# Optimization experiments

Hardware: AMD Instinct MI355X
Metric: run time of the kernel (lower is better)

## Reference

```python
import jax, jax.numpy as jnp
import numpy as np

B, T, F, H, BN = 131072, 20, 5, 32, 16


def _lstm_layer(x, Wih, Whh, bih, bhh):
    # x: [B, T, I]; Wih: [4H, I]; Whh: [4H, H]; biases: [4H]
    # PyTorch gate order: i, f, g, o
    b, h = x.shape[0], Whh.shape[1]
    x_t = jnp.swapaxes(x, 0, 1)                              # [T, B, I]
    pre = jnp.einsum('tbi,gi->tbg', x_t, Wih) + bih + bhh    # input contribution precomputed

    def step(carry, p):
        hprev, cprev = carry
        z = p + hprev @ Whh.T                                # [B, 4H]
        i, f, g, o = jnp.split(z, 4, axis=-1)
        i = jax.nn.sigmoid(i); f = jax.nn.sigmoid(f)
        g = jnp.tanh(g);       o = jax.nn.sigmoid(o)
        c = f * cprev + i * g
        hh = o * jnp.tanh(c)
        return (hh, c), hh

    h0 = jnp.zeros((b, h), x.dtype)
    (hT, cT), hs = jax.lax.scan(step, (h0, h0), pre)
    return jnp.swapaxes(hs, 0, 1), hT                        # [B, T, H], [B, H]


def setup_inputs() -> dict:
    key = jax.random.key(0)
    ks = jax.random.split(key, 24)
    k = 1.0 / np.sqrt(H)
    u = lambda kk, shp: jax.random.uniform(kk, shp, jnp.float32, -k, k)
    d = {
        'x': jax.random.normal(ks[0], (B, T, F), jnp.float32),
        # encoder layer 0 (input F) and layer 1 (input H)
        'enc_Wih0': u(ks[1], (4 * H, F)),  'enc_Whh0': u(ks[2], (4 * H, H)),
        'enc_bih0': u(ks[3], (4 * H,)),    'enc_bhh0': u(ks[4], (4 * H,)),
        'enc_Wih1': u(ks[5], (4 * H, H)),  'enc_Whh1': u(ks[6], (4 * H, H)),
        'enc_bih1': u(ks[7], (4 * H,)),    'enc_bhh1': u(ks[8], (4 * H,)),
        # bottleneck / expand MLPs
        'bn_W': u(ks[9], (BN, H)),  'bn_b': u(ks[10], (BN,)),
        'ex_W': u(ks[11], (H, BN)), 'ex_b': u(ks[12], (H,)),
        # decoder layers (both input H)
        'dec_Wih0': u(ks[13], (4 * H, H)), 'dec_Whh0': u(ks[14], (4 * H, H)),
        'dec_bih0': u(ks[15], (4 * H,)),   'dec_bhh0': u(ks[16], (4 * H,)),
        'dec_Wih1': u(ks[17], (4 * H, H)), 'dec_Whh1': u(ks[18], (4 * H, H)),
        'dec_bih1': u(ks[19], (4 * H,)),   'dec_bhh1': u(ks[20], (4 * H,)),
        # output projection
        'out_W': u(ks[21], (F, H)), 'out_b': u(ks[22], (F,)),
    }
    return d


def reference(x, enc_Wih0, enc_Whh0, enc_bih0, enc_bhh0,
              enc_Wih1, enc_Whh1, enc_bih1, enc_bhh1,
              bn_W, bn_b, ex_W, ex_b,
              dec_Wih0, dec_Whh0, dec_bih0, dec_bhh0,
              dec_Wih1, dec_Whh1, dec_bih1, dec_bhh1,
              out_W, out_b):
    # encoder (dropout inactive at inference)
    h0_seq, _ = _lstm_layer(x, enc_Wih0, enc_Whh0, enc_bih0, enc_bhh0)
    _, last_hidden = _lstm_layer(h0_seq, enc_Wih1, enc_Whh1, enc_bih1, enc_bhh1)
    latent = jax.nn.relu(last_hidden @ bn_W.T + bn_b)        # [B, BN]
    expanded = jax.nn.relu(latent @ ex_W.T + ex_b)           # [B, H]
    dec_in = jnp.broadcast_to(expanded[:, None, :], (expanded.shape[0], T, H))
    d0_seq, _ = _lstm_layer(dec_in, dec_Wih0, dec_Whh0, dec_bih0, dec_bhh0)
    d1_seq, _ = _lstm_layer(d0_seq, dec_Wih1, dec_Whh1, dec_bih1, dec_bhh1)
    return jnp.einsum('bth,fh->btf', d1_seq, out_W) + out_b  # [B, T, F]
```

## Files before the change

kernel.cpp:

```cpp
#include <hip/hip_runtime.h>

typedef float    f32x4 __attribute__((ext_vector_type(4)));
typedef _Float16 f16x8 __attribute__((ext_vector_type(8)));

#define BATCH 131072
#define SEQT  20
#define L1F  1.4426950408889634f
#define L2F  2.8853900817779268f

__device__ __forceinline__ float fexp2(float x){ return __builtin_amdgcn_exp2f(x); }
__device__ __forceinline__ float frcp (float x){ return __builtin_amdgcn_rcpf(x); }

__device__ __forceinline__ f32x4 MFMA(f16x8 a, f16x8 b, f32x4 c){
  return __builtin_amdgcn_mfma_f32_16x16x32_f16(a, b, c, 0, 0, 0);
}
__device__ __forceinline__ f16x8 zero8h(){
  f16x8 z;
#pragma unroll
  for (int e=0;e<8;++e) z[e]=(_Float16)0.f;
  return z;
}

__device__ __forceinline__ f16x8 pack8h(f32x4 lo, f32x4 hi, float sc){
  f16x8 f;
#pragma unroll
  for (int e=0;e<4;++e){ f[e] = (_Float16)(sc*lo[e]); f[4+e] = (_Float16)(sc*hi[e]); }
  return f;
}
__device__ __forceinline__ f16x8 gfragH(const float* __restrict__ W, int row, int kg, float sc){
  f32x4 lo = *(const f32x4*)(W + row*32 + 4*kg);
  f32x4 hi = *(const f32x4*)(W + row*32 + 16 + 4*kg);
  return pack8h(lo, hi, sc);
}
__device__ __forceinline__ f32x4 ld4(const float* __restrict__ p){ return *(const f32x4*)p; }

__device__ __forceinline__ void activate(const f32x4* acc, float* cs, f16x8& ph){
  float hv[8];
#pragma unroll
  for (int mm=0; mm<2; ++mm)
#pragma unroll
  for (int r=0; r<4; ++r){
    const int e = mm*4 + r;
    float zi = acc[0+mm][r];
    float zf = acc[2+mm][r];
    float zg = acc[4+mm][r];
    float zo = acc[6+mm][r];
    float A  = fexp2(-zi);
    float F  = fexp2(-zf);
    float B  = fexp2(zg);
    float ab = (1.0f+A)*(B+1.0f);
    float fp = 1.0f+F;
    float r1 = frcp(ab*fp);
    float cn = fmaf(ab*r1, cs[e], (B-1.0f)*fp*r1);
    cs[e] = cn;
    float E  = fexp2(-zo);
    float D  = fexp2(L2F*cn);
    hv[e] = (D-1.0f)*frcp((1.0f+E)*(D+1.0f));
  }
  f16x8 P;
#pragma unroll
  for (int e=0;e<8;++e) P[e] = (_Float16)hv[e];
  ph = P;
}

__global__ __launch_bounds__(256, 3) void lstm_ae_mfma(
    const float* __restrict__ x,
    const float* __restrict__ eWih0, const float* __restrict__ eWhh0,
    const float* __restrict__ ebih0, const float* __restrict__ ebhh0,
    const float* __restrict__ eWih1, const float* __restrict__ eWhh1,
    const float* __restrict__ ebih1, const float* __restrict__ ebhh1,
    const float* __restrict__ bnW,   const float* __restrict__ bnB,
    const float* __restrict__ exW,   const float* __restrict__ exB,
    const float* __restrict__ dWih0, const float* __restrict__ dWhh0,
    const float* __restrict__ dbih0, const float* __restrict__ dbhh0,
    const float* __restrict__ dWih1, const float* __restrict__ dWhh1,
    const float* __restrict__ dbih1, const float* __restrict__ dbhh1,
    const float* __restrict__ outW,  const float* __restrict__ outB,
    float* __restrict__ out)
{
  const int tid  = threadIdx.x;
  const int lane = tid & 63;
  const int w    = tid >> 6;
  const int cl   = lane & 15;
  const int kg   = lane >> 4;

  __shared__ __align__(16) float    sb[592];
  __shared__ __align__(16) _Float16 sfrag[13312];
  __shared__ __align__(16) float    sout[3200];

  if (tid < 128){
    float sc = (tid >= 64 && tid < 96) ? L2F : L1F;
    sb[128 + tid] = sc*(ebih1[tid] + ebhh1[tid]);
    sb[384 + tid] = sc*(dbih1[tid] + dbhh1[tid]);
  }
  if (tid < 16) sb[512 + tid] = (tid < 5) ? outB[tid] : 0.0f;
  if (tid < 16) sb[576 + tid] = 0.0f;

#pragma unroll
  for (int q=0; q<6; ++q){
    int tile = w + 4*q;
    int mat  = tile >> 3, m = tile & 7;
    float sc = (m==4 || m==5) ? L2F : L1F;
    const float* Wm = (mat==0) ? eWhh0 : (mat==1) ? eWih1 : eWhh1;
    f16x8 f = gfragH(Wm, m*16+cl, kg, sc);
    *(f16x8*)&sfrag[(mat*512 + m*64 + lane)*8] = f;
  }
  if (tid < 128){
    int m = tid >> 4, r = tid & 15;
    float sc = (m==4 || m==5) ? L2F : L1F;
    int row = m*16 + r;
    float b  = sc*(ebih0[row] + ebhh0[row]);
    _Float16 bh = (_Float16)b;
    float bl = b - (float)bh;
    f16x8 f;
#pragma unroll
    for (int e=0;e<5;++e) f[e] = (_Float16)(sc*eWih0[row*5+e]);
    f[5] = bh; f[6] = (_Float16)bl; f[7] = (_Float16)0.f;
    *(f16x8*)&sfrag[(1536 + m*16 + r)*8] = f;
  }
  __syncthreads();

  f32x4 rb1[8];
#pragma unroll
  for (int m=0;m<8;++m) rb1[m] = *(const f32x4*)&sb[128 + m*16 + kg*4];

  f32x4 acc[8], accB[8];
  float cs0[8], cs1[8];
#pragma unroll
  for (int e=0;e<8;++e){ cs0[e]=0.f; cs1[e]=0.f; }
  f16x8 ph0 = zero8h(), ph1 = zero8h();

  const _Float16* wih0p = (kg==0) ? &sfrag[(1536 + cl)*8] : (const _Float16*)&sb[576];
  const unsigned wih0s = (kg==0) ? 128u : 0u;

  const long blockb = (long)blockIdx.x * 64;
  const float* __restrict__ xcol = x + (blockb + (w*16+cl))*100;

  f16x8 xf = zero8h();
  if (kg==0){
    f16x8 X;
    X[0]=(_Float16)xcol[0]; X[1]=(_Float16)xcol[1]; X[2]=(_Float16)xcol[2];
    X[3]=(_Float16)xcol[3]; X[4]=(_Float16)xcol[4];
    X[5]=(_Float16)1.f; X[6]=(_Float16)1.f; X[7]=(_Float16)0.f;
    xf = X;
  }
#pragma unroll
  for (int m=0; m<8; ++m){
    const f16x8 fb = *(const f16x8*)&wih0p[m*wih0s];
    f32x4 b = {0.f,0.f,0.f,0.f};
    acc[m] = MFMA(fb, xf, b);
  }
  activate(acc, cs0, ph0);
  float xv0=0.f,xv1=0.f,xv2=0.f,xv3=0.f,xv4=0.f;
  if (kg==0){ xv0=xcol[5]; xv1=xcol[6]; xv2=xcol[7]; xv3=xcol[8]; xv4=xcol[9]; }

#pragma unroll 1
  for (int t=0; t<SEQT-1; ++t){
    asm volatile("" ::: "memory");
    float xn0=0.f,xn1=0.f,xn2=0.f,xn3=0.f,xn4=0.f;
    if (kg==0 && t < SEQT-2){
      const float* xp = xcol + (t+2)*5;
      xn0=xp[0]; xn1=xp[1]; xn2=xp[2]; xn3=xp[3]; xn4=xp[4];
    }
#pragma unroll
    for (int m=0; m<8; ++m){
      const f16x8 fd = *(const f16x8*)&sfrag[(1024 + m*64 + lane)*8];
      const f16x8 fc = *(const f16x8*)&sfrag[( 512 + m*64 + lane)*8];
      f32x4 b = rb1[m];
      b = MFMA(fd, ph1, b);
      b = MFMA(fc, ph0, b);
      accB[m] = b;
    }
    if (kg==0){
      f16x8 X;
      X[0]=(_Float16)xv0; X[1]=(_Float16)xv1; X[2]=(_Float16)xv2;
      X[3]=(_Float16)xv3; X[4]=(_Float16)xv4;
      X[5]=(_Float16)1.f; X[6]=(_Float16)1.f; X[7]=(_Float16)0.f;
      xf = X;
    }
#pragma unroll
    for (int m=0; m<8; ++m){
      const f16x8 fa = *(const f16x8*)&sfrag[(m*64 + lane)*8];
      const f16x8 fb = *(const f16x8*)&wih0p[m*wih0s];
      f32x4 b = {0.f,0.f,0.f,0.f};
      b = MFMA(fa, ph0, b);
      b = MFMA(fb, xf , b);
      acc[m] = b;
    }
    activate(accB, cs1, ph1);
    activate(acc,  cs0, ph0);
    xv0=xn0; xv1=xn1; xv2=xn2; xv3=xn3; xv4=xn4;
  }
  {
#pragma unroll
    for (int m=0; m<8; ++m){
      const f16x8 fd = *(const f16x8*)&sfrag[(1024 + m*64 + lane)*8];
      const f16x8 fc = *(const f16x8*)&sfrag[( 512 + m*64 + lane)*8];
      f32x4 b = rb1[m];
      b = MFMA(fd, ph1, b);
      b = MFMA(fc, ph0, b);
      accB[m] = b;
    }
    activate(accB, cs1, ph1);
  }
  __syncthreads();

#pragma unroll
  for (int q=0; q<6; ++q){
    int tile = w + 4*q;
    int mat  = tile >> 3, m = tile & 7;
    float sc = (m==4 || m==5) ? L2F : L1F;
    const float* Wm = (mat==0) ? dWhh0 : (mat==1) ? dWih1 : dWhh1;
    f16x8 f = gfragH(Wm, m*16+cl, kg, sc);
    *(f16x8*)&sfrag[(mat*512 + m*64 + lane)*8] = f;
  }
  if (tid < 64){
    int r2 = tid & 15, k2 = tid >> 4;
    f16x8 f = (r2 < 5) ? gfragH(outW, r2, k2, 1.0f) : zero8h();
    *(f16x8*)&sfrag[(1536 + tid)*8] = f;
  }

  f32x4 dpre[8];
  {
    f16x8 WBN = gfragH(bnW, cl, kg, 1.0f);
    f32x4 aL = ld4(bnB + kg*4);
    aL = MFMA(WBN, ph1, aL);
    f16x8 ltf = zero8h();
#pragma unroll
    for (int r=0; r<4; ++r) ltf[r] = (_Float16)fmaxf(aL[r], 0.0f);
    f32x4 aE[2];
#pragma unroll
    for (int mm=0; mm<2; ++mm){
      const int row = mm*16 + cl;
      f32x4 we = ld4(exW + row*16 + 4*kg);
      f16x8 X = zero8h();
#pragma unroll
      for (int e=0;e<4;++e) X[e] = (_Float16)we[e];
      f32x4 b = ld4(exB + mm*16 + kg*4);
      aE[mm] = MFMA(X, ltf, b);
    }
    f16x8 exf;
#pragma unroll
    for (int e=0; e<8; ++e) exf[e] = (_Float16)fmaxf(aE[e>>2][e&3], 0.0f);
#pragma unroll
    for (int m=0; m<8; ++m){
      const float sc = (m==4 || m==5) ? L2F : L1F;
      f16x8 wm = gfragH(dWih0, m*16+cl, kg, sc);
      f32x4 b = sc*( ld4(dbih0 + m*16 + kg*4) + ld4(dbhh0 + m*16 + kg*4) );
      dpre[m] = MFMA(wm, exf, b);
    }
  }

#pragma unroll
  for (int e=0;e<8;++e){ cs0[e]=0.f; cs1[e]=0.f; }
  ph0 = zero8h(); ph1 = zero8h();

  __syncthreads();
#pragma unroll
  for (int m=0;m<8;++m) rb1[m] = *(const f32x4*)&sb[384 + m*16 + kg*4];

  const f32x4 obias = *(const f32x4*)&sb[512 + kg*4];
  float* __restrict__ ob = out + blockb*100;
  const int sobase = (w*16 + cl)*50;

  activate(dpre, cs0, ph0);

#pragma unroll 1
  for (int t=0; t<SEQT-1; ++t){
    asm volatile("" ::: "memory");
#pragma unroll
    for (int m=0; m<8; ++m){
      const f16x8 fd = *(const f16x8*)&sfrag[(1024 + m*64 + lane)*8];
      const f16x8 fc = *(const f16x8*)&sfrag[( 512 + m*64 + lane)*8];
      f32x4 b = rb1[m];
      b = MFMA(fd, ph1, b);
      b = MFMA(fc, ph0, b);
      accB[m] = b;
    }
#pragma unroll
    for (int m=0; m<8; ++m){
      const f16x8 fa = *(const f16x8*)&sfrag[(m*64 + lane)*8];
      acc[m] = MFMA(fa, ph0, dpre[m]);
    }
    activate(accB, cs1, ph1);
    const f16x8 fo = *(const f16x8*)&sfrag[(1536 + lane)*8];
    f32x4 o = MFMA(fo, ph1, obias);
    activate(acc, cs0, ph0);
    int ts = (t >= 10) ? t-10 : t;
    if (kg == 0){
      sout[sobase + ts*5 + 0] = o[0];
      sout[sobase + ts*5 + 1] = o[1];
      sout[sobase + ts*5 + 2] = o[2];
      sout[sobase + ts*5 + 3] = o[3];
    } else if (kg == 1){
      sout[sobase + ts*5 + 4] = o[0];
    }
    if (t == 9){
      __syncthreads();
      for (int i=tid; i<3200; i+=256){
        int bb = i/50, off = i - bb*50;
        ob[bb*100 + off] = sout[i];
      }
      __syncthreads();
    }
  }
  {
#pragma unroll
    for (int m=0; m<8; ++m){
      const f16x8 fd = *(const f16x8*)&sfrag[(1024 + m*64 + lane)*8];
      const f16x8 fc = *(const f16x8*)&sfrag[( 512 + m*64 + lane)*8];
      f32x4 b = rb1[m];
      b = MFMA(fd, ph1, b);
      b = MFMA(fc, ph0, b);
      accB[m] = b;
    }
    activate(accB, cs1, ph1);
    const f16x8 fo = *(const f16x8*)&sfrag[(1536 + lane)*8];
    f32x4 o = MFMA(fo, ph1, obias);
    if (kg == 0){
      sout[sobase + 45 + 0] = o[0];
      sout[sobase + 45 + 1] = o[1];
      sout[sobase + 45 + 2] = o[2];
      sout[sobase + 45 + 3] = o[3];
    } else if (kg == 1){
      sout[sobase + 45 + 4] = o[0];
    }
  }
  __syncthreads();
  for (int i=tid; i<3200; i+=256){
    int bb = i/50, off = i - bb*50;
    ob[bb*100 + 50 + off] = sout[i];
  }
}

extern "C" void kernel_launch(void* const* d_in, const int* in_sizes, int n_in,
                              void* d_out, int out_size, void* d_ws, size_t ws_size,
                              hipStream_t stream)
{
  const float* x     = (const float*)d_in[0];
  const float* eWih0 = (const float*)d_in[1];
  const float* eWhh0 = (const float*)d_in[2];
  const float* ebih0 = (const float*)d_in[3];
  const float* ebhh0 = (const float*)d_in[4];
  const float* eWih1 = (const float*)d_in[5];
  const float* eWhh1 = (const float*)d_in[6];
  const float* ebih1 = (const float*)d_in[7];
  const float* ebhh1 = (const float*)d_in[8];
  const float* bnW   = (const float*)d_in[9];
  const float* bnB   = (const float*)d_in[10];
  const float* exW   = (const float*)d_in[11];
  const float* exB   = (const float*)d_in[12];
  const float* dWih0 = (const float*)d_in[13];
  const float* dWhh0 = (const float*)d_in[14];
  const float* dbih0 = (const float*)d_in[15];
  const float* dbhh0 = (const float*)d_in[16];
  const float* dWih1 = (const float*)d_in[17];
  const float* dWhh1 = (const float*)d_in[18];
  const float* dbih1 = (const float*)d_in[19];
  const float* dbhh1 = (const float*)d_in[20];
  const float* outW  = (const float*)d_in[21];
  const float* outB  = (const float*)d_in[22];

  dim3 grid(BATCH / 64), block(256);
  hipLaunchKernelGGL(lstm_ae_mfma, grid, block, 0, stream,
                     x,
                     eWih0, eWhh0, ebih0, ebhh0,
                     eWih1, eWhh1, ebih1, ebhh1,
                     bnW, bnB, exW, exB,
                     dWih0, dWhh0, dbih0, dbhh0,
                     dWih1, dWhh1, dbih1, dbhh1,
                     outW, outB,
                     (float*)d_out);
}
```

Before: 339.8 us.

## Shrink LDS footprint and raise occupancy to four blocks per CU

Cuts shared memory use so four 256-thread blocks fit per CU, and raises the launch-bounds minimum from 3 to 4. To make room, the encoder layer-0 input fragments and the output-projection fragment now live in registers instead of LDS, the output staging buffer holds 8 timesteps and is flushed three times instead of twice, and one FMA is folded in the cell-state update. The aim is more concurrent waves to hide MFMA and transcendental latency, at the cost of tighter register limits that may cause spills, plus one extra barrier-synchronised flush phase.

```diff
diff --git a/kernel.cpp b/kernel.cpp
--- a/kernel.cpp
+++ b/kernel.cpp
@@ -51,7 +51,7 @@
     float ab = (1.0f+A)*(B+1.0f);
     float fp = 1.0f+F;
     float r1 = frcp(ab*fp);
-    float cn = fmaf(ab*r1, cs[e], (B-1.0f)*fp*r1);
+    float cn = r1 * fmaf(ab, cs[e], fmaf(B, fp, -fp));
     cs[e] = cn;
     float E  = fexp2(-zo);
     float D  = fexp2(L2F*cn);
@@ -63,7 +63,7 @@
   ph = P;
 }
 
-__global__ __launch_bounds__(256, 3) void lstm_ae_mfma(
+__global__ __launch_bounds__(256, 4) void lstm_ae_mfma(
     const float* __restrict__ x,
     const float* __restrict__ eWih0, const float* __restrict__ eWhh0,
     const float* __restrict__ ebih0, const float* __restrict__ ebhh0,
@@ -84,17 +84,16 @@
   const int cl   = lane & 15;
   const int kg   = lane >> 4;
 
-  __shared__ __align__(16) float    sb[592];
-  __shared__ __align__(16) _Float16 sfrag[13312];
-  __shared__ __align__(16) float    sout[3200];
+  __shared__ __align__(16) float    sb[272];
+  __shared__ __align__(16) _Float16 sfrag[12288];
+  __shared__ __align__(16) float    sout[2560];
 
   if (tid < 128){
     float sc = (tid >= 64 && tid < 96) ? L2F : L1F;
-    sb[128 + tid] = sc*(ebih1[tid] + ebhh1[tid]);
-    sb[384 + tid] = sc*(dbih1[tid] + dbhh1[tid]);
-  }
-  if (tid < 16) sb[512 + tid] = (tid < 5) ? outB[tid] : 0.0f;
-  if (tid < 16) sb[576 + tid] = 0.0f;
+    sb[      tid] = sc*(ebih1[tid] + ebhh1[tid]);
+    sb[128 + tid] = sc*(dbih1[tid] + dbhh1[tid]);
+  }
+  if (tid < 16) sb[256 + tid] = (tid < 5) ? outB[tid] : 0.0f;
 
 #pragma unroll
   for (int q=0; q<6; ++q){
@@ -105,33 +104,36 @@
     f16x8 f = gfragH(Wm, m*16+cl, kg, sc);
     *(f16x8*)&sfrag[(mat*512 + m*64 + lane)*8] = f;
   }
-  if (tid < 128){
-    int m = tid >> 4, r = tid & 15;
-    float sc = (m==4 || m==5) ? L2F : L1F;
-    int row = m*16 + r;
-    float b  = sc*(ebih0[row] + ebhh0[row]);
-    _Float16 bh = (_Float16)b;
-    float bl = b - (float)bh;
-    f16x8 f;
-#pragma unroll
-    for (int e=0;e<5;++e) f[e] = (_Float16)(sc*eWih0[row*5+e]);
-    f[5] = bh; f[6] = (_Float16)bl; f[7] = (_Float16)0.f;
-    *(f16x8*)&sfrag[(1536 + m*16 + r)*8] = f;
+
+  f16x8 fB[8];
+#pragma unroll
+  for (int m=0; m<8; ++m){
+    if (kg == 0){
+      const float sc = (m==4 || m==5) ? L2F : L1F;
+      const int row = m*16 + cl;
+      float b  = sc*(ebih0[row] + ebhh0[row]);
+      _Float16 bh = (_Float16)b;
+      float bl = b - (float)bh;
+      f16x8 f;
+#pragma unroll
+      for (int e=0;e<5;++e) f[e] = (_Float16)(sc*eWih0[row*5+e]);
+      f[5] = bh; f[6] = (_Float16)bl; f[7] = (_Float16)0.f;
+      fB[m] = f;
+    } else {
+      fB[m] = zero8h();
+    }
   }
   __syncthreads();
 
   f32x4 rb1[8];
 #pragma unroll
-  for (int m=0;m<8;++m) rb1[m] = *(const f32x4*)&sb[128 + m*16 + kg*4];
+  for (int m=0;m<8;++m) rb1[m] = *(const f32x4*)&sb[m*16 + kg*4];
 
   f32x4 acc[8], accB[8];
   float cs0[8], cs1[8];
 #pragma unroll
   for (int e=0;e<8;++e){ cs0[e]=0.f; cs1[e]=0.f; }
   f16x8 ph0 = zero8h(), ph1 = zero8h();
-
-  const _Float16* wih0p = (kg==0) ? &sfrag[(1536 + cl)*8] : (const _Float16*)&sb[576];
-  const unsigned wih0s = (kg==0) ? 128u : 0u;
 
   const long blockb = (long)blockIdx.x * 64;
   const float* __restrict__ xcol = x + (blockb + (w*16+cl))*100;
@@ -146,9 +148,8 @@
   }
 #pragma unroll
   for (int m=0; m<8; ++m){
-    const f16x8 fb = *(const f16x8*)&wih0p[m*wih0s];
     f32x4 b = {0.f,0.f,0.f,0.f};
-    acc[m] = MFMA(fb, xf, b);
+    acc[m] = MFMA(fB[m], xf, b);
   }
   activate(acc, cs0, ph0);
   float xv0=0.f,xv1=0.f,xv2=0.f,xv3=0.f,xv4=0.f;
@@ -181,10 +182,9 @@
 #pragma unroll
     for (int m=0; m<8; ++m){
       const f16x8 fa = *(const f16x8*)&sfrag[(m*64 + lane)*8];
-      const f16x8 fb = *(const f16x8*)&wih0p[m*wih0s];
       f32x4 b = {0.f,0.f,0.f,0.f};
       b = MFMA(fa, ph0, b);
-      b = MFMA(fb, xf , b);
+      b = MFMA(fB[m], xf, b);
       acc[m] = b;
     }
     activate(accB, cs1, ph1);
@@ -214,11 +214,7 @@
     f16x8 f = gfragH(Wm, m*16+cl, kg, sc);
     *(f16x8*)&sfrag[(mat*512 + m*64 + lane)*8] = f;
   }
-  if (tid < 64){
-    int r2 = tid & 15, k2 = tid >> 4;
-    f16x8 f = (r2 < 5) ? gfragH(outW, r2, k2, 1.0f) : zero8h();
-    *(f16x8*)&sfrag[(1536 + tid)*8] = f;
-  }
+  const f16x8 fo = (cl < 5) ? gfragH(outW, cl, kg, 1.0f) : zero8h();
 
   f32x4 dpre[8];
   {
@@ -257,11 +253,11 @@
 
   __syncthreads();
 #pragma unroll
-  for (int m=0;m<8;++m) rb1[m] = *(const f32x4*)&sb[384 + m*16 + kg*4];
-
-  const f32x4 obias = *(const f32x4*)&sb[512 + kg*4];
+  for (int m=0;m<8;++m) rb1[m] = *(const f32x4*)&sb[128 + m*16 + kg*4];
+
+  const f32x4 obias = *(const f32x4*)&sb[256 + kg*4];
   float* __restrict__ ob = out + blockb*100;
-  const int sobase = (w*16 + cl)*50;
+  const int sobase = (w*16 + cl)*40;
 
   activate(dpre, cs0, ph0);
 
@@ -283,10 +279,9 @@
       acc[m] = MFMA(fa, ph0, dpre[m]);
     }
     activate(accB, cs1, ph1);
-    const f16x8 fo = *(const f16x8*)&sfrag[(1536 + lane)*8];
     f32x4 o = MFMA(fo, ph1, obias);
     activate(acc, cs0, ph0);
-    int ts = (t >= 10) ? t-10 : t;
+    int ts = t - (t >= 16 ? 16 : (t >= 8 ? 8 : 0));
     if (kg == 0){
       sout[sobase + ts*5 + 0] = o[0];
       sout[sobase + ts*5 + 1] = o[1];
@@ -295,11 +290,19 @@
     } else if (kg == 1){
       sout[sobase + ts*5 + 4] = o[0];
     }
-    if (t == 9){
+    if (t == 7){
       __syncthreads();
-      for (int i=tid; i<3200; i+=256){
-        int bb = i/50, off = i - bb*50;
+      for (int i=tid; i<2560; i+=256){
+        int bb = i/40, off = i - bb*40;
         ob[bb*100 + off] = sout[i];
+      }
+      __syncthreads();
+    }
+    if (t == 15){
+      __syncthreads();
+      for (int i=tid; i<2560; i+=256){
+        int bb = i/40, off = i - bb*40;
+        ob[bb*100 + 40 + off] = sout[i];
       }
       __syncthreads();
     }
@@ -315,21 +318,20 @@
       accB[m] = b;
     }
     activate(accB, cs1, ph1);
-    const f16x8 fo = *(const f16x8*)&sfrag[(1536 + lane)*8];
     f32x4 o = MFMA(fo, ph1, obias);
     if (kg == 0){
-      sout[sobase + 45 + 0] = o[0];
-      sout[sobase + 45 + 1] = o[1];
-      sout[sobase + 45 + 2] = o[2];
-      sout[sobase + 45 + 3] = o[3];
+      sout[sobase + 15 + 0] = o[0];
+      sout[sobase + 15 + 1] = o[1];
+      sout[sobase + 15 + 2] = o[2];
+      sout[sobase + 15 + 3] = o[3];
     } else if (kg == 1){
-      sout[sobase + 45 + 4] = o[0];
+      sout[sobase + 15 + 4] = o[0];
     }
   }
   __syncthreads();
-  for (int i=tid; i<3200; i+=256){
-    int bb = i/50, off = i - bb*50;
-    ob[bb*100 + 50 + off] = sout[i];
+  for (int i=tid; i<1280; i+=256){
+    int bb = i/20, off = i - bb*20;
+    ob[bb*100 + 80 + off] = sout[bb*40 + off];
   }
 }
 
```

New measurement: 786.7 us. 2.31x slower.
